# Kernel tuning notes

Hardware: AMD Instinct MI355X
Metric: run time of the kernel (lower is better)

## Reference

```python
import jax, jax.numpy as jnp
import numpy as np

N_NODES = 50000
N_EDGES = 800000
F_IN = 128
HEADS = 2
C_HID = 64
N_GRAPHS = 32
NEG_SLOPE = 0.2
LP_LAYERS = 2
LP_ALPHA = 0.5


def gatv2_conv(x, src, dst, W_l, W_r, att, bias):
    """GATv2Conv (concat=True), edge_attr=None, self-loops already in src/dst."""
    H, C = att.shape
    N = x.shape[0]
    xl = (x @ W_l).reshape(N, H, C)  # source-side transform (x_j)
    xr = (x @ W_r).reshape(N, H, C)  # target-side transform (x_i)
    xj = xl[src]                      # [E,H,C]
    e = jax.nn.leaky_relu(xr[dst] + xj, NEG_SLOPE)
    logits = jnp.einsum('ehc,hc->eh', e, att)  # [E,H]
    # segment softmax over incoming edges of each target node
    m = jax.ops.segment_max(logits, dst, num_segments=N)
    m = jnp.where(jnp.isfinite(m), m, 0.0)
    p = jnp.exp(logits - m[dst])
    s = jax.ops.segment_sum(p, dst, num_segments=N)
    alpha = p / (s[dst] + 1e-16)
    out = jax.ops.segment_sum(xj * alpha[:, :, None], dst, num_segments=N)
    return out.reshape(N, H * C) + bias


def label_prop(y, src, dst):
    """PyG LabelPropagation: sym gcn_norm (no self-loops), clamp(0,1) post-step."""
    N = y.shape[0]
    ones = jnp.ones(src.shape[0], dtype=y.dtype)
    deg = jax.ops.segment_sum(ones, dst, num_segments=N)
    dinv = jnp.where(deg > 0, jax.lax.rsqrt(jnp.maximum(deg, 1.0)), 0.0)
    w = (dinv[src] * dinv[dst])[:, None]
    res = (1.0 - LP_ALPHA) * y
    out = y
    for _ in range(LP_LAYERS):
        out = LP_ALPHA * jax.ops.segment_sum(out[src] * w, dst, num_segments=N) + res
        out = jnp.clip(out, 0.0, 1.0)
    return out


def setup_inputs() -> dict:
    key = jax.random.key(0)
    ks = jax.random.split(key, 16)
    HC = HEADS * C_HID

    def glorot(k, shape):
        lim = np.sqrt(6.0 / (shape[0] + shape[-1]))
        return jax.random.uniform(k, shape, jnp.float32, -lim, lim)

    x = jax.random.normal(ks[0], (N_NODES, F_IN), jnp.float32)
    edge_index = jax.random.randint(ks[1], (2, N_EDGES), 0, N_NODES, jnp.int32)
    batch = jnp.sort(jax.random.randint(ks[2], (N_NODES,), 0, N_GRAPHS, jnp.int32))
    return {
        'x': x, 'edge_index': edge_index, 'batch': batch,
        'W_l1': glorot(ks[3], (F_IN, HC)), 'W_r1': glorot(ks[4], (F_IN, HC)),
        'att1': glorot(ks[5], (HEADS, C_HID)), 'b1': jnp.zeros((HC,), jnp.float32),
        'W_l2': glorot(ks[6], (HC, HC)), 'W_r2': glorot(ks[7], (HC, HC)),
        'att2': glorot(ks[8], (HEADS, C_HID)), 'b2': jnp.zeros((HC,), jnp.float32),
        'mlp_W1': glorot(ks[9], (F_IN + 2 * HC, 256)), 'mlp_b1': jnp.zeros((256,), jnp.float32),
        'mlp_W2': glorot(ks[10], (256, 128)), 'mlp_b2': jnp.zeros((128,), jnp.float32),
    }


def reference(x, edge_index, batch, W_l1, W_r1, att1, b1, W_l2, W_r2, att2, b2,
              mlp_W1, mlp_b1, mlp_W2, mlp_b2):
    N = x.shape[0]
    src, dst = edge_index[0], edge_index[1]
    # GATv2Conv adds self-loops by default
    loop = jnp.arange(N, dtype=src.dtype)
    src_sl = jnp.concatenate([src, loop])
    dst_sl = jnp.concatenate([dst, loop])

    h0 = x
    h1 = jax.nn.elu(gatv2_conv(h0, src_sl, dst_sl, W_l1, W_r1, att1, b1))
    h1 = label_prop(h1, src, dst)
    h2 = jax.nn.elu(gatv2_conv(h1, src_sl, dst_sl, W_l2, W_r2, att2, b2))
    h2 = label_prop(h2, src, dst)

    combined = jnp.concatenate([h0, h1, h2], axis=-1)  # [N, 384]
    # global mean pool over graphs
    sums = jax.ops.segment_sum(combined, batch, num_segments=N_GRAPHS)
    cnts = jax.ops.segment_sum(jnp.ones((N,), combined.dtype), batch, num_segments=N_GRAPHS)
    g = sums / jnp.maximum(cnts, 1.0)[:, None]  # [G, 384]

    h = jax.nn.relu(g @ mlp_W1 + mlp_b1)  # dropout is identity in eval
    return h @ mlp_W2 + mlp_b2
```

## Files before the change

kernel.cpp:

```cpp
#include <hip/hip_runtime.h>
#include <math.h>

#define FDIM 128
#define NEG_SLOPE 0.2f
#define LP_ALPHA 0.5f
#define NGRAPHS 32
#define POOLF 384
#define MLP_H 256
#define OUT_F 128
#define POOL_CH 8

#define LRELU(z) ((z) > 0.0f ? (z) : NEG_SLOPE * (z))
#define RFL(v) __builtin_amdgcn_readfirstlane(v)

__global__ void count_deg_k(const int* __restrict__ dst, int* __restrict__ deg, int E) {
    int e = blockIdx.x * blockDim.x + threadIdx.x;
    if (e < E) atomicAdd(&deg[dst[e]], 1);
}

__global__ void scan_excl_k(const int* __restrict__ deg, int* __restrict__ row_ptr, int n) {
    __shared__ int part[1024];
    int tid = threadIdx.x;
    int chunk = (n + 1023) >> 10;
    int s0 = tid * chunk;
    int s1 = min(s0 + chunk, n);
    int sum = 0;
    for (int i = s0; i < s1; ++i) sum += deg[i];
    part[tid] = sum;
    __syncthreads();
    for (int off = 1; off < 1024; off <<= 1) {
        int v = (tid >= off) ? part[tid - off] : 0;
        __syncthreads();
        part[tid] += v;
        __syncthreads();
    }
    int run = (tid == 0) ? 0 : part[tid - 1];
    for (int i = s0; i < s1; ++i) { row_ptr[i] = run; run += deg[i]; }
    if (tid == 1023) row_ptr[n] = part[1023];
}

__global__ void dinv_k(const int* __restrict__ deg, float* __restrict__ dinv, int N) {
    int i = blockIdx.x * blockDim.x + threadIdx.x;
    if (i < N) {
        int d = deg[i];
        dinv[i] = (d > 0) ? (1.0f / sqrtf((float)d)) : 0.0f;
    }
}

__global__ void scatter_k(const int* __restrict__ src, const int* __restrict__ dst,
                          const int* __restrict__ row_ptr, int* __restrict__ fill,
                          const float* __restrict__ dinv, int2* __restrict__ elist, int E) {
    int e = blockIdx.x * blockDim.x + threadIdx.x;
    if (e >= E) return;
    int d = dst[e], s = src[e];
    int pos = atomicAdd(&fill[d], 1);
    elist[row_ptr[d] + pos] = make_int2(s, __float_as_int(dinv[s]));
}

__global__ void gbound_k(const int* __restrict__ batch, int* __restrict__ gb, int N) {
    int g = threadIdx.x;
    if (g > NGRAPHS) return;
    int lo = 0, hi = N;
    while (lo < hi) {
        int mid = (lo + hi) >> 1;
        if (batch[mid] < g) lo = mid + 1; else hi = mid;
    }
    gb[g] = lo;
}

__global__ __launch_bounds__(256) void gemm128_k(const float* __restrict__ X,
                                                 const float* __restrict__ W,
                                                 float* __restrict__ Y, int N) {
    __shared__ float Xs[FDIM][68];
    int t = threadIdx.x;
    int r0 = blockIdx.x * 64;
    for (int idx = t; idx < 64 * FDIM; idx += 256) {
        int k = idx & 127, r = idx >> 7;
        int row = r0 + r;
        Xs[k][r] = (row < N) ? X[(size_t)row * FDIM + k] : 0.0f;
    }
    __syncthreads();
    int tr = t >> 5;
    int tc = t & 31;
    float acc[8][4];
#pragma unroll
    for (int r = 0; r < 8; ++r)
#pragma unroll
        for (int c = 0; c < 4; ++c) acc[r][c] = 0.0f;

#pragma unroll 2
    for (int k = 0; k < FDIM; ++k) {
        float4 b = *(const float4*)(W + k * FDIM + tc * 4);
        float4 a0 = *(const float4*)(&Xs[k][tr * 8]);
        float4 a1 = *(const float4*)(&Xs[k][tr * 8 + 4]);
        float av[8] = {a0.x, a0.y, a0.z, a0.w, a1.x, a1.y, a1.z, a1.w};
#pragma unroll
        for (int r = 0; r < 8; ++r) {
            acc[r][0] = fmaf(av[r], b.x, acc[r][0]);
            acc[r][1] = fmaf(av[r], b.y, acc[r][1]);
            acc[r][2] = fmaf(av[r], b.z, acc[r][2]);
            acc[r][3] = fmaf(av[r], b.w, acc[r][3]);
        }
    }
#pragma unroll
    for (int r = 0; r < 8; ++r) {
        int row = r0 + tr * 8 + r;
        if (row < N) {
            float4 o = make_float4(acc[r][0], acc[r][1], acc[r][2], acc[r][3]);
            *(float4*)(Y + (size_t)row * FDIM + tc * 4) = o;
        }
    }
}

__global__ __launch_bounds__(256) void gat_pull_k(const float* __restrict__ xl,
                                                  const float* __restrict__ xr,
                                                  const int* __restrict__ row_ptr,
                                                  const int2* __restrict__ elist,
                                                  const float* __restrict__ att,
                                                  const float* __restrict__ bias,
                                                  float* __restrict__ out, int N) {
    int wid = threadIdx.x >> 6;
    int lane = threadIdx.x & 63;
    int i = blockIdx.x * 4 + wid;
    if (i >= N) return;
    float2 at  = *(const float2*)(att + 2 * lane);
    size_t ibase = (size_t)i * FDIM + 2 * lane;
    float2 xrv   = *(const float2*)(xr + ibase);
    float2 xself = *(const float2*)(xl + ibase);

    auto hred = [](float v) {
        v += __shfl_xor(v, 16, 64);
        v += __shfl_xor(v, 8, 64);
        v += __shfl_xor(v, 4, 64);
        v += __shfl_xor(v, 2, 64);
        v += __shfl_xor(v, 1, 64);
        return v;
    };

    float lself = hred(LRELU(xrv.x + xself.x) * at.x + LRELU(xrv.y + xself.y) * at.y);
    float m0 = lself, s0 = 1.0f, a0x = xself.x, a0y = xself.y;
    float m1 = -INFINITY, s1 = 0.0f, a1x = 0.0f, a1y = 0.0f;

    int beg = row_ptr[i], end = row_ptr[i + 1];
    int p = beg;
    for (; p + 3 < end; p += 4) {
        int j0 = RFL(elist[p].x);
        int j1 = RFL(elist[p + 1].x);
        int j2 = RFL(elist[p + 2].x);
        int j3 = RFL(elist[p + 3].x);
        float2 x0 = *(const float2*)(xl + (size_t)j0 * FDIM + 2 * lane);
        float2 x1 = *(const float2*)(xl + (size_t)j1 * FDIM + 2 * lane);
        float2 x2 = *(const float2*)(xl + (size_t)j2 * FDIM + 2 * lane);
        float2 x3 = *(const float2*)(xl + (size_t)j3 * FDIM + 2 * lane);
        float l0 = hred(LRELU(xrv.x + x0.x) * at.x + LRELU(xrv.y + x0.y) * at.y);
        float l1 = hred(LRELU(xrv.x + x1.x) * at.x + LRELU(xrv.y + x1.y) * at.y);
        float l2 = hred(LRELU(xrv.x + x2.x) * at.x + LRELU(xrv.y + x2.y) * at.y);
        float l3 = hred(LRELU(xrv.x + x3.x) * at.x + LRELU(xrv.y + x3.y) * at.y);
        { float mn = fmaxf(m0, l0); float sc = __expf(m0 - mn), pe = __expf(l0 - mn);
          s0 = fmaf(s0, sc, pe); a0x = fmaf(a0x, sc, pe * x0.x); a0y = fmaf(a0y, sc, pe * x0.y); m0 = mn; }
        { float mn = fmaxf(m1, l1); float sc = __expf(m1 - mn), pe = __expf(l1 - mn);
          s1 = fmaf(s1, sc, pe); a1x = fmaf(a1x, sc, pe * x1.x); a1y = fmaf(a1y, sc, pe * x1.y); m1 = mn; }
        { float mn = fmaxf(m0, l2); float sc = __expf(m0 - mn), pe = __expf(l2 - mn);
          s0 = fmaf(s0, sc, pe); a0x = fmaf(a0x, sc, pe * x2.x); a0y = fmaf(a0y, sc, pe * x2.y); m0 = mn; }
        { float mn = fmaxf(m1, l3); float sc = __expf(m1 - mn), pe = __expf(l3 - mn);
          s1 = fmaf(s1, sc, pe); a1x = fmaf(a1x, sc, pe * x3.x); a1y = fmaf(a1y, sc, pe * x3.y); m1 = mn; }
    }
    for (; p < end; ++p) {
        int j0 = RFL(elist[p].x);
        float2 x0 = *(const float2*)(xl + (size_t)j0 * FDIM + 2 * lane);
        float l0 = hred(LRELU(xrv.x + x0.x) * at.x + LRELU(xrv.y + x0.y) * at.y);
        float mn = fmaxf(m0, l0); float sc = __expf(m0 - mn), pe = __expf(l0 - mn);
        s0 = fmaf(s0, sc, pe); a0x = fmaf(a0x, sc, pe * x0.x); a0y = fmaf(a0y, sc, pe * x0.y); m0 = mn;
    }
    float mn = fmaxf(m0, m1);
    float c0 = __expf(m0 - mn);
    float c1 = (m1 == -INFINITY) ? 0.0f : __expf(m1 - mn);
    float s = fmaf(s0, c0, s1 * c1) + 1e-16f;
    float rx = (a0x * c0 + a1x * c1) / s;
    float ry = (a0y * c0 + a1y * c1) / s;
    float2 bv = *(const float2*)(bias + 2 * lane);
    float zx = rx + bv.x, zy = ry + bv.y;
    float2 o;
    o.x = (zx > 0.0f) ? zx : (__expf(zx) - 1.0f);
    o.y = (zy > 0.0f) ? zy : (__expf(zy) - 1.0f);
    *(float2*)(out + ibase) = o;
}

__global__ __launch_bounds__(256) void lp_pull_k(const float* __restrict__ y,
                                                 const float* __restrict__ cur,
                                                 float* __restrict__ nxt,
                                                 const int* __restrict__ row_ptr,
                                                 const int2* __restrict__ elist,
                                                 const float* __restrict__ dinv, int N) {
    int wid = threadIdx.x >> 6, lane = threadIdx.x & 63;
    int i = blockIdx.x * 4 + wid;
    if (i >= N) return;
    int beg = row_ptr[i], end = row_ptr[i + 1];
    float ax0 = 0.f, ay0 = 0.f, ax1 = 0.f, ay1 = 0.f;
    float ax2 = 0.f, ay2 = 0.f, ax3 = 0.f, ay3 = 0.f;
    float ax4 = 0.f, ay4 = 0.f, ax5 = 0.f, ay5 = 0.f;
    float ax6 = 0.f, ay6 = 0.f, ax7 = 0.f, ay7 = 0.f;
    int p = beg;
    for (; p + 7 < end; p += 8) {
        int2 e0 = elist[p + 0], e1 = elist[p + 1], e2 = elist[p + 2], e3 = elist[p + 3];
        int2 e4 = elist[p + 4], e5 = elist[p + 5], e6 = elist[p + 6], e7 = elist[p + 7];
        int j0 = RFL(e0.x); float w0 = __int_as_float(RFL(e0.y));
        int j1 = RFL(e1.x); float w1 = __int_as_float(RFL(e1.y));
        int j2 = RFL(e2.x); float w2 = __int_as_float(RFL(e2.y));
        int j3 = RFL(e3.x); float w3 = __int_as_float(RFL(e3.y));
        int j4 = RFL(e4.x); float w4 = __int_as_float(RFL(e4.y));
        int j5 = RFL(e5.x); float w5 = __int_as_float(RFL(e5.y));
        int j6 = RFL(e6.x); float w6 = __int_as_float(RFL(e6.y));
        int j7 = RFL(e7.x); float w7 = __int_as_float(RFL(e7.y));
        float2 v0 = *(const float2*)(cur + (size_t)j0 * FDIM + 2 * lane);
        float2 v1 = *(const float2*)(cur + (size_t)j1 * FDIM + 2 * lane);
        float2 v2 = *(const float2*)(cur + (size_t)j2 * FDIM + 2 * lane);
        float2 v3 = *(const float2*)(cur + (size_t)j3 * FDIM + 2 * lane);
        float2 v4 = *(const float2*)(cur + (size_t)j4 * FDIM + 2 * lane);
        float2 v5 = *(const float2*)(cur + (size_t)j5 * FDIM + 2 * lane);
        float2 v6 = *(const float2*)(cur + (size_t)j6 * FDIM + 2 * lane);
        float2 v7 = *(const float2*)(cur + (size_t)j7 * FDIM + 2 * lane);
        ax0 = fmaf(w0, v0.x, ax0); ay0 = fmaf(w0, v0.y, ay0);
        ax1 = fmaf(w1, v1.x, ax1); ay1 = fmaf(w1, v1.y, ay1);
        ax2 = fmaf(w2, v2.x, ax2); ay2 = fmaf(w2, v2.y, ay2);
        ax3 = fmaf(w3, v3.x, ax3); ay3 = fmaf(w3, v3.y, ay3);
        ax4 = fmaf(w4, v4.x, ax4); ay4 = fmaf(w4, v4.y, ay4);
        ax5 = fmaf(w5, v5.x, ax5); ay5 = fmaf(w5, v5.y, ay5);
        ax6 = fmaf(w6, v6.x, ax6); ay6 = fmaf(w6, v6.y, ay6);
        ax7 = fmaf(w7, v7.x, ax7); ay7 = fmaf(w7, v7.y, ay7);
    }
    for (; p < end; ++p) {
        int2 e0 = elist[p];
        int j0 = RFL(e0.x); float w0 = __int_as_float(RFL(e0.y));
        float2 v0 = *(const float2*)(cur + (size_t)j0 * FDIM + 2 * lane);
        ax0 = fmaf(w0, v0.x, ax0); ay0 = fmaf(w0, v0.y, ay0);
    }
    float sx = ((ax0 + ax1) + (ax2 + ax3)) + ((ax4 + ax5) + (ax6 + ax7));
    float sy = ((ay0 + ay1) + (ay2 + ay3)) + ((ay4 + ay5) + (ay6 + ay7));
    float di = dinv[i];
    float2 yv = *(const float2*)(y + (size_t)i * FDIM + 2 * lane);
    float vx = LP_ALPHA * (di * sx) + (1.0f - LP_ALPHA) * yv.x;
    float vy = LP_ALPHA * (di * sy) + (1.0f - LP_ALPHA) * yv.y;
    float2 o;
    o.x = fminf(fmaxf(vx, 0.f), 1.f);
    o.y = fminf(fmaxf(vy, 0.f), 1.f);
    *(float2*)(nxt + (size_t)i * FDIM + 2 * lane) = o;
}

__global__ void pool_part_k(const float* __restrict__ x, const float* __restrict__ h1,
                            const float* __restrict__ h2, const int* __restrict__ gb,
                            float* __restrict__ part) {
    int g = blockIdx.x, si = blockIdx.y, ch = blockIdx.z;
    int t = threadIdx.x;
    const float* s = (si == 0) ? x : ((si == 1) ? h1 : h2);
    int n0g = gb[g], n1g = gb[g + 1];
    int len = n1g - n0g;
    int per = (len + POOL_CH - 1) / POOL_CH;
    int n0 = n0g + ch * per;
    int n1 = min(n0 + per, n1g);
    float acc = 0.0f;
    for (int n = n0; n < n1; ++n) acc += s[(size_t)n * FDIM + t];
    part[(((g * 3 + si) << 3) + ch) * FDIM + t] = acc;
}

__global__ void mlp1_k(const float* __restrict__ part, const int* __restrict__ gb,
                       const float* __restrict__ W1, const float* __restrict__ b1,
                       float* __restrict__ h) {
    int g = blockIdx.x;
    int t = threadIdx.x;
    __shared__ float gm[POOLF];
    int cnt = gb[g + 1] - gb[g];
    float inv = 1.0f / fmaxf((float)cnt, 1.0f);
    for (int f = t; f < POOLF; f += 256) {
        int si = f >> 7, fl = f & 127;
        float s = 0.0f;
#pragma unroll
        for (int c = 0; c < POOL_CH; ++c)
            s += part[(((g * 3 + si) << 3) + c) * FDIM + fl];
        gm[f] = s * inv;
    }
    __syncthreads();
    float acc = b1[t];
    for (int k = 0; k < POOLF; ++k) acc = fmaf(gm[k], W1[k * MLP_H + t], acc);
    h[g * MLP_H + t] = fmaxf(acc, 0.0f);
}

__global__ void mlp2_k(const float* __restrict__ h, const float* __restrict__ W2,
                       const float* __restrict__ b2, float* __restrict__ out) {
    int g = blockIdx.x;
    int t = threadIdx.x;
    __shared__ float hs[MLP_H];
    for (int k = t; k < MLP_H; k += 128) hs[k] = h[g * MLP_H + k];
    __syncthreads();
    float acc = b2[t];
    for (int k = 0; k < MLP_H; ++k) acc = fmaf(hs[k], W2[k * OUT_F + t], acc);
    out[g * OUT_F + t] = acc;
}

extern "C" void kernel_launch(void* const* d_in, const int* in_sizes, int n_in,
                              void* d_out, int out_size, void* d_ws, size_t ws_size,
                              hipStream_t stream) {
    const float* x    = (const float*)d_in[0];
    const int*   ei   = (const int*)d_in[1];
    const int*   batch= (const int*)d_in[2];
    const float* W_l1 = (const float*)d_in[3];
    const float* W_r1 = (const float*)d_in[4];
    const float* att1 = (const float*)d_in[5];
    const float* b1   = (const float*)d_in[6];
    const float* W_l2 = (const float*)d_in[7];
    const float* W_r2 = (const float*)d_in[8];
    const float* att2 = (const float*)d_in[9];
    const float* b2   = (const float*)d_in[10];
    const float* mW1  = (const float*)d_in[11];
    const float* mb1  = (const float*)d_in[12];
    const float* mW2  = (const float*)d_in[13];
    const float* mb2  = (const float*)d_in[14];
    float* out = (float*)d_out;

    const int N = in_sizes[2];
    const int E = in_sizes[1] / 2;
    const int* src = ei;
    const int* dst = ei + E;

    char* w = (char*)d_ws;
    auto alloc = [&](size_t bytes) -> char* {
        char* p = w;
        w += (bytes + 255) & ~(size_t)255;
        return p;
    };
    float* bufA = (float*)alloc((size_t)N * FDIM * 4);
    float* bufB = (float*)alloc((size_t)N * FDIM * 4);
    float* bufC = (float*)alloc((size_t)N * FDIM * 4);
    float* bufD = (float*)alloc((size_t)N * FDIM * 4);
    int* deg     = (int*)alloc((size_t)N * 4);
    int* fill    = (int*)alloc((size_t)N * 4);
    int* row_lp  = (int*)alloc((size_t)(N + 1) * 4);
    int2* elist  = (int2*)alloc((size_t)E * 8);
    float* dinv  = (float*)alloc((size_t)N * 4);
    int* gb      = (int*)alloc((size_t)(NGRAPHS + 1) * 4);
    float* part  = (float*)alloc((size_t)NGRAPHS * 3 * POOL_CH * FDIM * 4);
    float* mlp_h = (float*)alloc((size_t)NGRAPHS * MLP_H * 4);

    const int TB = 256;
    int gE = (E + TB - 1) / TB;
    int gN = (N + TB - 1) / TB;

    hipMemsetAsync(deg, 0, (size_t)N * 4, stream);
    hipMemsetAsync(fill, 0, (size_t)N * 4, stream);
    count_deg_k<<<gE, TB, 0, stream>>>(dst, deg, E);
    gbound_k<<<1, 64, 0, stream>>>(batch, gb, N);
    scan_excl_k<<<1, 1024, 0, stream>>>(deg, row_lp, N);
    dinv_k<<<gN, TB, 0, stream>>>(deg, dinv, N);
    scatter_k<<<gE, TB, 0, stream>>>(src, dst, row_lp, fill, dinv, elist, E);

    int gGemm = (N + 63) / 64;
    int gWave = (N + 3) / 4;

    gemm128_k<<<gGemm, 256, 0, stream>>>(x, W_l1, bufA, N);
    gemm128_k<<<gGemm, 256, 0, stream>>>(x, W_r1, bufB, N);
    gat_pull_k<<<gWave, 256, 0, stream>>>(bufA, bufB, row_lp, elist, att1, b1, bufC, N);
    lp_pull_k<<<gWave, 256, 0, stream>>>(bufC, bufC, bufA, row_lp, elist, dinv, N);
    lp_pull_k<<<gWave, 256, 0, stream>>>(bufC, bufA, bufC, row_lp, elist, dinv, N);

    gemm128_k<<<gGemm, 256, 0, stream>>>(bufC, W_l2, bufA, N);
    gemm128_k<<<gGemm, 256, 0, stream>>>(bufC, W_r2, bufB, N);
    gat_pull_k<<<gWave, 256, 0, stream>>>(bufA, bufB, row_lp, elist, att2, b2, bufD, N);
    lp_pull_k<<<gWave, 256, 0, stream>>>(bufD, bufD, bufA, row_lp, elist, dinv, N);
    lp_pull_k<<<gWave, 256, 0, stream>>>(bufD, bufA, bufD, row_lp, elist, dinv, N);

    pool_part_k<<<dim3(NGRAPHS, 3, POOL_CH), 128, 0, stream>>>(x, bufC, bufD, gb, part);

    mlp1_k<<<NGRAPHS, 256, 0, stream>>>(part, gb, mW1, mb1, mlp_h);
    mlp2_k<<<NGRAPHS, 128, 0, stream>>>(mlp_h, mW2, mb2, out);
}
```

Baseline: 863.3 us.

## Parallelize degree scan, fuse dinv, merge dual GEMMs, nontemporal elist stores

Replaces the single-block 1024-thread serial-chunk scan with a three-kernel tiled parallel scan (tile sums, tile offsets, per-tile write) and folds the dinv computation into the final scan pass. The two per-layer GEMMs (W_l and W_r) are merged into one kernel that loads the X tile into shared memory once and computes both outputs. Scatter writes CSR entries with nontemporal 64-bit stores. The scan targets a serial single-block bottleneck. The fused GEMM doubles accumulator registers, which may lower occupancy. The tile-offset scan uses a single 64-lane wave, so it assumes at most 64 tiles (about 65K nodes).

After: 773.5 us. -10.4%, faster.

```diff
diff --git a/kernel.cpp b/kernel.cpp
--- a/kernel.cpp
+++ b/kernel.cpp
@@ -18,33 +18,70 @@
     if (e < E) atomicAdd(&deg[dst[e]], 1);
 }
 
-__global__ void scan_excl_k(const int* __restrict__ deg, int* __restrict__ row_ptr, int n) {
-    __shared__ int part[1024];
-    int tid = threadIdx.x;
-    int chunk = (n + 1023) >> 10;
-    int s0 = tid * chunk;
-    int s1 = min(s0 + chunk, n);
-    int sum = 0;
-    for (int i = s0; i < s1; ++i) sum += deg[i];
-    part[tid] = sum;
+__global__ __launch_bounds__(256) void scan_part_k(const int* __restrict__ deg,
+                                                   int* __restrict__ tileSum, int N) {
+    int b = blockIdx.x, t = threadIdx.x;
+    int base = b * 1024 + t * 4;
+    int v = 0;
+    if (base + 3 < N) { int4 d = *(const int4*)(deg + base); v = d.x + d.y + d.z + d.w; }
+    else if (base < N) {
+        v = deg[base];
+        if (base + 1 < N) v += deg[base + 1];
+        if (base + 2 < N) v += deg[base + 2];
+    }
+#pragma unroll
+    for (int off = 32; off > 0; off >>= 1) v += __shfl_xor(v, off, 64);
+    __shared__ int ws[4];
+    if ((t & 63) == 0) ws[t >> 6] = v;
     __syncthreads();
-    for (int off = 1; off < 1024; off <<= 1) {
-        int v = (tid >= off) ? part[tid - off] : 0;
-        __syncthreads();
-        part[tid] += v;
-        __syncthreads();
-    }
-    int run = (tid == 0) ? 0 : part[tid - 1];
-    for (int i = s0; i < s1; ++i) { row_ptr[i] = run; run += deg[i]; }
-    if (tid == 1023) row_ptr[n] = part[1023];
-}
-
-__global__ void dinv_k(const int* __restrict__ deg, float* __restrict__ dinv, int N) {
-    int i = blockIdx.x * blockDim.x + threadIdx.x;
-    if (i < N) {
-        int d = deg[i];
-        dinv[i] = (d > 0) ? (1.0f / sqrtf((float)d)) : 0.0f;
-    }
+    if (t == 0) tileSum[b] = ws[0] + ws[1] + ws[2] + ws[3];
+}
+
+__global__ void scan_tiles_k(const int* __restrict__ tileSum, int* __restrict__ tileOff, int nt) {
+    int t = threadIdx.x;
+    int v = (t < nt) ? tileSum[t] : 0;
+    int incl = v;
+#pragma unroll
+    for (int off = 1; off < 64; off <<= 1) {
+        int u = __shfl_up(incl, off, 64);
+        if (t >= off) incl += u;
+    }
+    if (t < nt) tileOff[t] = incl - v;
+}
+
+__global__ __launch_bounds__(256) void scan_write_k(const int* __restrict__ deg,
+                                                    const int* __restrict__ tileOff,
+                                                    int* __restrict__ row_ptr,
+                                                    float* __restrict__ dinv, int N, int E) {
+    int b = blockIdx.x, t = threadIdx.x;
+    int base = b * 1024 + t * 4;
+    int d0 = 0, d1 = 0, d2 = 0, d3 = 0;
+    if (base + 3 < N) { int4 d = *(const int4*)(deg + base); d0 = d.x; d1 = d.y; d2 = d.z; d3 = d.w; }
+    else if (base < N) {
+        d0 = deg[base];
+        if (base + 1 < N) d1 = deg[base + 1];
+        if (base + 2 < N) d2 = deg[base + 2];
+    }
+    int lsum = d0 + d1 + d2 + d3;
+    int lane = t & 63, wv = t >> 6;
+    int incl = lsum;
+#pragma unroll
+    for (int off = 1; off < 64; off <<= 1) {
+        int u = __shfl_up(incl, off, 64);
+        if (lane >= off) incl += u;
+    }
+    __shared__ int wsum[4];
+    if (lane == 63) wsum[wv] = incl;
+    __syncthreads();
+    int woff = 0;
+#pragma unroll
+    for (int k = 0; k < 4; ++k) if (k < wv) woff += wsum[k];
+    int off0 = tileOff[b] + woff + (incl - lsum);
+    if (base < N)     { row_ptr[base]     = off0;                dinv[base]     = d0 > 0 ? 1.0f / sqrtf((float)d0) : 0.0f; }
+    if (base + 1 < N) { row_ptr[base + 1] = off0 + d0;           dinv[base + 1] = d1 > 0 ? 1.0f / sqrtf((float)d1) : 0.0f; }
+    if (base + 2 < N) { row_ptr[base + 2] = off0 + d0 + d1;      dinv[base + 2] = d2 > 0 ? 1.0f / sqrtf((float)d2) : 0.0f; }
+    if (base + 3 < N) { row_ptr[base + 3] = off0 + d0 + d1 + d2; dinv[base + 3] = d3 > 0 ? 1.0f / sqrtf((float)d3) : 0.0f; }
+    if (b == 0 && t == 0) row_ptr[N] = E;
 }
 
 __global__ void scatter_k(const int* __restrict__ src, const int* __restrict__ dst,
@@ -54,7 +91,9 @@
     if (e >= E) return;
     int d = dst[e], s = src[e];
     int pos = atomicAdd(&fill[d], 1);
-    elist[row_ptr[d] + pos] = make_int2(s, __float_as_int(dinv[s]));
+    unsigned long long v = (unsigned int)s |
+                           ((unsigned long long)(unsigned int)__float_as_int(dinv[s]) << 32);
+    __builtin_nontemporal_store(v, (unsigned long long*)&elist[row_ptr[d] + pos]);
 }
 
 __global__ void gbound_k(const int* __restrict__ batch, int* __restrict__ gb, int N) {
@@ -68,9 +107,11 @@
     gb[g] = lo;
 }
 
-__global__ __launch_bounds__(256) void gemm128_k(const float* __restrict__ X,
-                                                 const float* __restrict__ W,
-                                                 float* __restrict__ Y, int N) {
+__global__ __launch_bounds__(256) void gemm128x2_k(const float* __restrict__ X,
+                                                   const float* __restrict__ Wl,
+                                                   const float* __restrict__ Wr,
+                                                   float* __restrict__ Yl,
+                                                   float* __restrict__ Yr, int N) {
     __shared__ float Xs[FDIM][68];
     int t = threadIdx.x;
     int r0 = blockIdx.x * 64;
@@ -82,32 +123,34 @@
     __syncthreads();
     int tr = t >> 5;
     int tc = t & 31;
-    float acc[8][4];
-#pragma unroll
-    for (int r = 0; r < 8; ++r)
-#pragma unroll
-        for (int c = 0; c < 4; ++c) acc[r][c] = 0.0f;
-
+    float accl[8][4] = {{0.f}}, accr[8][4] = {{0.f}};
 #pragma unroll 2
     for (int k = 0; k < FDIM; ++k) {
-        float4 b = *(const float4*)(W + k * FDIM + tc * 4);
+        float4 bl = *(const float4*)(Wl + k * FDIM + tc * 4);
+        float4 br = *(const float4*)(Wr + k * FDIM + tc * 4);
         float4 a0 = *(const float4*)(&Xs[k][tr * 8]);
         float4 a1 = *(const float4*)(&Xs[k][tr * 8 + 4]);
         float av[8] = {a0.x, a0.y, a0.z, a0.w, a1.x, a1.y, a1.z, a1.w};
 #pragma unroll
         for (int r = 0; r < 8; ++r) {
-            acc[r][0] = fmaf(av[r], b.x, acc[r][0]);
-            acc[r][1] = fmaf(av[r], b.y, acc[r][1]);
-            acc[r][2] = fmaf(av[r], b.z, acc[r][2]);
-            acc[r][3] = fmaf(av[r], b.w, acc[r][3]);
+            accl[r][0] = fmaf(av[r], bl.x, accl[r][0]);
+            accl[r][1] = fmaf(av[r], bl.y, accl[r][1]);
+            accl[r][2] = fmaf(av[r], bl.z, accl[r][2]);
+            accl[r][3] = fmaf(av[r], bl.w, accl[r][3]);
+            accr[r][0] = fmaf(av[r], br.x, accr[r][0]);
+            accr[r][1] = fmaf(av[r], br.y, accr[r][1]);
+            accr[r][2] = fmaf(av[r], br.z, accr[r][2]);
+            accr[r][3] = fmaf(av[r], br.w, accr[r][3]);
         }
     }
 #pragma unroll
     for (int r = 0; r < 8; ++r) {
         int row = r0 + tr * 8 + r;
         if (row < N) {
-            float4 o = make_float4(acc[r][0], acc[r][1], acc[r][2], acc[r][3]);
-            *(float4*)(Y + (size_t)row * FDIM + tc * 4) = o;
+            *(float4*)(Yl + (size_t)row * FDIM + tc * 4) =
+                make_float4(accl[r][0], accl[r][1], accl[r][2], accl[r][3]);
+            *(float4*)(Yr + (size_t)row * FDIM + tc * 4) =
+                make_float4(accr[r][0], accr[r][1], accr[r][2], accr[r][3]);
         }
     }
 }
@@ -338,32 +381,33 @@
     int2* elist  = (int2*)alloc((size_t)E * 8);
     float* dinv  = (float*)alloc((size_t)N * 4);
     int* gb      = (int*)alloc((size_t)(NGRAPHS + 1) * 4);
+    int* tileSum = (int*)alloc((size_t)64 * 4);
+    int* tileOff = (int*)alloc((size_t)64 * 4);
     float* part  = (float*)alloc((size_t)NGRAPHS * 3 * POOL_CH * FDIM * 4);
     float* mlp_h = (float*)alloc((size_t)NGRAPHS * MLP_H * 4);
 
     const int TB = 256;
     int gE = (E + TB - 1) / TB;
-    int gN = (N + TB - 1) / TB;
+    int nTiles = (N + 1023) / 1024;
 
     hipMemsetAsync(deg, 0, (size_t)N * 4, stream);
     hipMemsetAsync(fill, 0, (size_t)N * 4, stream);
     count_deg_k<<<gE, TB, 0, stream>>>(dst, deg, E);
     gbound_k<<<1, 64, 0, stream>>>(batch, gb, N);
-    scan_excl_k<<<1, 1024, 0, stream>>>(deg, row_lp, N);
-    dinv_k<<<gN, TB, 0, stream>>>(deg, dinv, N);
+    scan_part_k<<<nTiles, 256, 0, stream>>>(deg, tileSum, N);
+    scan_tiles_k<<<1, 64, 0, stream>>>(tileSum, tileOff, nTiles);
+    scan_write_k<<<nTiles, 256, 0, stream>>>(deg, tileOff, row_lp, dinv, N, E);
     scatter_k<<<gE, TB, 0, stream>>>(src, dst, row_lp, fill, dinv, elist, E);
 
     int gGemm = (N + 63) / 64;
     int gWave = (N + 3) / 4;
 
-    gemm128_k<<<gGemm, 256, 0, stream>>>(x, W_l1, bufA, N);
-    gemm128_k<<<gGemm, 256, 0, stream>>>(x, W_r1, bufB, N);
+    gemm128x2_k<<<gGemm, 256, 0, stream>>>(x, W_l1, W_r1, bufA, bufB, N);
     gat_pull_k<<<gWave, 256, 0, stream>>>(bufA, bufB, row_lp, elist, att1, b1, bufC, N);
     lp_pull_k<<<gWave, 256, 0, stream>>>(bufC, bufC, bufA, row_lp, elist, dinv, N);
     lp_pull_k<<<gWave, 256, 0, stream>>>(bufC, bufA, bufC, row_lp, elist, dinv, N);
 
-    gemm128_k<<<gGemm, 256, 0, stream>>>(bufC, W_l2, bufA, N);
-    gemm128_k<<<gGemm, 256, 0, stream>>>(bufC, W_r2, bufB, N);
+    gemm128x2_k<<<gGemm, 256, 0, stream>>>(bufC, W_l2, W_r2, bufA, bufB, N);
     gat_pull_k<<<gWave, 256, 0, stream>>>(bufA, bufB, row_lp, elist, att2, b2, bufD, N);
     lp_pull_k<<<gWave, 256, 0, stream>>>(bufD, bufD, bufA, row_lp, elist, dinv, N);
     lp_pull_k<<<gWave, 256, 0, stream>>>(bufD, bufA, bufD, row_lp, elist, dinv, N);
```
